# Optimization experiments

Hardware: AMD Instinct MI355X
Metric: run time of the kernel (lower is better)

Reference implementation:

```python
import jax, jax.numpy as jnp
import numpy as np

N = 50000
E = 1_600_000
IN_C, HID_C, OUT_C = 128, 64, 16
NEG_SLOPE = 0.2


def setup_inputs() -> dict:
    key = jax.random.key(0)
    ks = jax.random.split(key, 16)
    x = jax.random.normal(ks[0], (N, IN_C), dtype=jnp.float32)
    edge_index = jax.random.randint(ks[1], (2, E), 0, N, dtype=jnp.int32)
    edge_weight = jax.random.uniform(ks[2], (E,), dtype=jnp.float32)

    def lin(k, fan_in, fan_out):
        s = (6.0 / (fan_in + fan_out)) ** 0.5
        return jax.random.uniform(k, (fan_in, fan_out), jnp.float32, -s, s)

    params = {
        "W1": lin(ks[3], IN_C, HID_C),
        "a_src1": jax.random.normal(ks[4], (HID_C,), jnp.float32) * 0.1,
        "a_dst1": jax.random.normal(ks[5], (HID_C,), jnp.float32) * 0.1,
        "b1": jnp.zeros((HID_C,), jnp.float32),
        "W2": lin(ks[6], HID_C, HID_C),
        "a_src2": jax.random.normal(ks[7], (HID_C,), jnp.float32) * 0.1,
        "a_dst2": jax.random.normal(ks[8], (HID_C,), jnp.float32) * 0.1,
        "b2": jnp.zeros((HID_C,), jnp.float32),
        "W3": lin(ks[9], HID_C, OUT_C),
        "a_src3": jax.random.normal(ks[10], (OUT_C,), jnp.float32) * 0.1,
        "a_dst3": jax.random.normal(ks[11], (OUT_C,), jnp.float32) * 0.1,
        "b3": jnp.zeros((OUT_C,), jnp.float32),
    }
    return {"x": x, "edge_index": edge_index, "edge_weight": edge_weight, **params}


def gat_conv(x, W, a_src, a_dst, b, src, dst):
    """Single-head PyG GATConv, add_self_loops=False, eval mode."""
    h = x @ W                                    # [N, C]
    alpha_src = (h * a_src).sum(-1)              # [N]
    alpha_dst = (h * a_dst).sum(-1)              # [N]
    e = jax.nn.leaky_relu(alpha_src[src] + alpha_dst[dst], NEG_SLOPE)  # [E]
    # softmax over incoming edges of each target node
    m = jax.ops.segment_max(e, dst, num_segments=N)
    e = jnp.exp(e - m[dst])
    denom = jax.ops.segment_sum(e, dst, num_segments=N)
    alpha = e / (denom[dst] + 1e-16)             # [E]
    out = jax.ops.segment_sum(h[src] * alpha[:, None], dst, num_segments=N)
    return out + b


def reference(x, edge_index, edge_weight,
              W1, a_src1, a_dst1, b1,
              W2, a_src2, a_dst2, b2,
              W3, a_src3, a_dst3, b3):
    src, dst = edge_index[0], edge_index[1]
    # edge_weight unused: GATConv has no lin_edge (edge_dim=None)
    h = jax.nn.relu(gat_conv(x, W1, a_src1, a_dst1, b1, src, dst))
    h = jax.nn.relu(gat_conv(h, W2, a_src2, a_dst2, b2, src, dst))
    return gat_conv(h, W3, a_src3, a_dst3, b3, src, dst)
```

## Files before the change

kernel.cpp:

```cpp
#include <hip/hip_runtime.h>
#include <hip/hip_fp16.h>
#include <math.h>

#define N_NODES 50000
#define N_EDGES 1600000
#define BSH 8
#define NBUCK ((N_NODES + 255) >> BSH)
#define EPB 2048
#define NBLK ((N_EDGES + EPB - 1) / EPB)


__global__ __launch_bounds__(256) void bucket_hist(const int* __restrict__ dst,
                                                   int* __restrict__ bhist_t, int e) {
    __shared__ int h[NBUCK];
    for (int i = threadIdx.x; i < NBUCK; i += 256) h[i] = 0;
    __syncthreads();
    int base = blockIdx.x * EPB;
#pragma unroll
    for (int j = 0; j < EPB / 256; ++j) {
        int i = base + j * 256 + threadIdx.x;
        if (i < e) atomicAdd(&h[dst[i] >> BSH], 1);
    }
    __syncthreads();
    for (int i = threadIdx.x; i < NBUCK; i += 256)
        bhist_t[i * NBLK + blockIdx.x] = h[i];
}

__global__ __launch_bounds__(256) void bucket_totals(const int* __restrict__ bhist_t,
                                                     int* __restrict__ btot) {
    int b = blockIdx.x;
    const int* col = bhist_t + (size_t)b * NBLK;
    int s = 0;
    for (int i = threadIdx.x; i < NBLK; i += 256) s += col[i];
#pragma unroll
    for (int off = 1; off < 64; off <<= 1) s += __shfl_xor(s, off);
    __shared__ int red[4];
    if ((threadIdx.x & 63) == 0) red[threadIdx.x >> 6] = s;
    __syncthreads();
    if (threadIdx.x == 0)
        btot[b] = red[0] + red[1] + red[2] + red[3];
}

__global__ __launch_bounds__(64) void rewrite_offsets(int* __restrict__ bhist_t,
                                                      const int* __restrict__ btot,
                                                      int* __restrict__ rowptr) {
    int b = blockIdx.x;
    int lane = threadIdx.x;
    int pre = 0;
    for (int i = lane; i < NBUCK; i += 64) if (i < b) pre += btot[i];
#pragma unroll
    for (int off = 1; off < 64; off <<= 1) pre += __shfl_xor(pre, off);
    if (b == 0 && lane == 0) rowptr[N_NODES] = N_EDGES;

    int* col = bhist_t + (size_t)b * NBLK;
    __shared__ int buf[NBLK];
    for (int i = lane; i < NBLK; i += 64) buf[i] = col[i];
    __syncthreads();
    constexpr int CH = (NBLK + 63) / 64;
    int lo = lane * CH;
    int hi = lo + CH; if (hi > NBLK) hi = NBLK;
    int s = 0;
    for (int i = lo; i < hi; ++i) s += buf[i];
    int inc = s;
#pragma unroll
    for (int off = 1; off < 64; off <<= 1) {
        int t = __shfl_up(inc, off);
        if (lane >= off) inc += t;
    }
    int run = pre + inc - s;
    for (int i = lo; i < hi; ++i) { int c = buf[i]; col[i] = run; run += c; }
}

__global__ __launch_bounds__(256) void bucket_scatter(const int* __restrict__ src,
                                                      const int* __restrict__ dst,
                                                      const int* __restrict__ bhist_t,
                                                      unsigned* __restrict__ packed, int e) {
    __shared__ int lcnt[NBUCK];
    __shared__ int lbase[NBUCK];
    __shared__ int gbase[NBUCK];
    __shared__ unsigned stage[EPB];
    __shared__ unsigned char sbk[EPB];
    __shared__ int wsum[4];
    int r = blockIdx.x;
    for (int i = threadIdx.x; i < NBUCK; i += 256) {
        lcnt[i] = 0;
        gbase[i] = bhist_t[i * NBLK + r];
    }
    __syncthreads();
    int base = r * EPB;
    int bk[EPB / 256], lrank[EPB / 256];
    unsigned pk[EPB / 256];
    bool val[EPB / 256];
#pragma unroll
    for (int j = 0; j < EPB / 256; ++j) {
        int i = base + j * 256 + threadIdx.x;
        val[j] = (i < e);
        if (val[j]) {
            int d = dst[i];
            bk[j] = d >> BSH;
            pk[j] = (unsigned)src[i] | ((unsigned)(d & ((1 << BSH) - 1)) << 16);
            lrank[j] = atomicAdd(&lcnt[bk[j]], 1);
        }
    }
    __syncthreads();
    {
        int lane = threadIdx.x & 63, w = threadIdx.x >> 6;
        int v = (threadIdx.x < NBUCK) ? lcnt[threadIdx.x] : 0;
        int inc = v;
#pragma unroll
        for (int off = 1; off < 64; off <<= 1) {
            int t = __shfl_up(inc, off);
            if (lane >= off) inc += t;
        }
        if (lane == 63) wsum[w] = inc;
        __syncthreads();
        int woff = 0;
#pragma unroll
        for (int k = 0; k < 3; ++k) if (k < w) woff += wsum[k];
        if (threadIdx.x < NBUCK) lbase[threadIdx.x] = woff + inc - v;
    }
    __syncthreads();
#pragma unroll
    for (int j = 0; j < EPB / 256; ++j) {
        if (val[j]) {
            int slot = lbase[bk[j]] + lrank[j];
            stage[slot] = pk[j];
            sbk[slot] = (unsigned char)bk[j];
        }
    }
    __syncthreads();
    int vn = e - base; if (vn > EPB) vn = EPB;
    for (int i = threadIdx.x; i < vn; i += 256) {
        int b = sbk[i];
        packed[gbase[b] + (i - lbase[b])] = stage[i];
    }
}

__global__ __launch_bounds__(512) void csr_finalize(const unsigned* __restrict__ packed,
                                                    const int* __restrict__ btot,
                                                    int* __restrict__ rowptr,
                                                    unsigned short* __restrict__ csr_src) {
    int b = blockIdx.x;
    __shared__ int sb[2];
    if (threadIdx.x < 64) {
        int pre = 0, tot = 0;
        for (int i = threadIdx.x; i < NBUCK; i += 64) {
            int v = btot[i];
            if (i < b) pre += v;
            if (i == b) tot = v;
        }
#pragma unroll
        for (int off = 1; off < 64; off <<= 1) {
            pre += __shfl_xor(pre, off);
            tot += __shfl_xor(tot, off);
        }
        if (threadIdx.x == 0) { sb[0] = pre; sb[1] = pre + tot; }
    }
    __syncthreads();
    int s0 = sb[0], s1 = sb[1];
    int cnt = s1 - s0;
    __shared__ int ncnt[256];
    __shared__ int ncur[256];
    __shared__ int wsum[4];
    if (threadIdx.x < 256) ncnt[threadIdx.x] = 0;
    __syncthreads();
    for (int i = threadIdx.x; i < cnt; i += 512)
        atomicAdd(&ncnt[packed[s0 + i] >> 16], 1);
    __syncthreads();
    int lane = threadIdx.x & 63, w = threadIdx.x >> 6;
    int v = 0, inc = 0;
    if (threadIdx.x < 256) {
        v = ncnt[threadIdx.x]; inc = v;
#pragma unroll
        for (int off = 1; off < 64; off <<= 1) {
            int t = __shfl_up(inc, off);
            if (lane >= off) inc += t;
        }
        if (lane == 63) wsum[w] = inc;
    }
    __syncthreads();
    if (threadIdx.x < 256) {
        int woff = 0;
#pragma unroll
        for (int k = 0; k < 3; ++k) if (k < w) woff += wsum[k];
        int excl = woff + inc - v;
        int node = (b << BSH) + threadIdx.x;
        if (node < N_NODES) rowptr[node] = s0 + excl;
        ncur[threadIdx.x] = s0 + excl;
    }
    __syncthreads();
    for (int i = threadIdx.x; i < cnt; i += 512) {
        unsigned p = packed[s0 + i];
        int pos = atomicAdd(&ncur[p >> 16], 1);
        csr_src[pos] = (unsigned short)(p & 0xFFFFu);
    }
}


template<int K, int C, bool IN_HALF, bool OUT_HALF>
__global__ __launch_bounds__(256) void gemm_alpha(
        const void* __restrict__ inv, const float* __restrict__ W,
        const float* __restrict__ a_src, const float* __restrict__ a_dst,
        void* __restrict__ hv, float* __restrict__ as_, float* __restrict__ ad_, int n)
{
    constexpr int CPT = C / 16;
    constexpr int KP = K + 4;
    __shared__ float sx[64][KP];
    __shared__ float sW[K * C];
    int row0 = blockIdx.x * 64;
    int nvalid = n - row0;

    if constexpr (IN_HALF) {
        const __half* inh = (const __half*)inv;
        for (int idx = threadIdx.x; idx < 64 * K / 8; idx += 256) {
            int r = idx / (K / 8), kc = idx % (K / 8);
            uint4 v = {0u, 0u, 0u, 0u};
            if (r < nvalid) v = *(const uint4*)&inh[(size_t)(row0 + r) * K + kc * 8];
            float2 f0 = __half22float2(*(__half2*)&v.x);
            float2 f1 = __half22float2(*(__half2*)&v.y);
            float2 f2 = __half22float2(*(__half2*)&v.z);
            float2 f3 = __half22float2(*(__half2*)&v.w);
            float* d = &sx[r][kc * 8];
            d[0] = f0.x; d[1] = f0.y; d[2] = f1.x; d[3] = f1.y;
            d[4] = f2.x; d[5] = f2.y; d[6] = f3.x; d[7] = f3.y;
        }
    } else {
        const float* in = (const float*)inv;
        for (int idx = threadIdx.x; idx < 64 * K / 4; idx += 256) {
            int r = idx / (K / 4), kc = idx % (K / 4);
            float4 v = {0, 0, 0, 0};
            if (r < nvalid) v = *(const float4*)&in[(size_t)(row0 + r) * K + kc * 4];
            *(float4*)&sx[r][kc * 4] = v;
        }
    }
    for (int idx = threadIdx.x; idx < K * C / 4; idx += 256)
        *(float4*)&sW[idx * 4] = *(const float4*)&W[idx * 4];
    __syncthreads();

    int g  = threadIdx.x >> 4;
    int ci = threadIdx.x & 15;
    int r0 = g * 4;
    int c0 = ci * CPT;

    if constexpr (CPT == 4) {
        float4 acc0 = {0,0,0,0}, acc1 = {0,0,0,0}, acc2 = {0,0,0,0}, acc3 = {0,0,0,0};
        for (int k = 0; k < K; k += 4) {
            float4 w0 = *(const float4*)&sW[(k + 0) * C + c0];
            float4 w1 = *(const float4*)&sW[(k + 1) * C + c0];
            float4 w2 = *(const float4*)&sW[(k + 2) * C + c0];
            float4 w3 = *(const float4*)&sW[(k + 3) * C + c0];
            float4 x0 = *(const float4*)&sx[r0 + 0][k];
            float4 x1 = *(const float4*)&sx[r0 + 1][k];
            float4 x2 = *(const float4*)&sx[r0 + 2][k];
            float4 x3 = *(const float4*)&sx[r0 + 3][k];
#define STEP(A, X) \
            A.x = fmaf(X.x, w0.x, A.x); A.y = fmaf(X.x, w0.y, A.y); \
            A.z = fmaf(X.x, w0.z, A.z); A.w = fmaf(X.x, w0.w, A.w); \
            A.x = fmaf(X.y, w1.x, A.x); A.y = fmaf(X.y, w1.y, A.y); \
            A.z = fmaf(X.y, w1.z, A.z); A.w = fmaf(X.y, w1.w, A.w); \
            A.x = fmaf(X.z, w2.x, A.x); A.y = fmaf(X.z, w2.y, A.y); \
            A.z = fmaf(X.z, w2.z, A.z); A.w = fmaf(X.z, w2.w, A.w); \
            A.x = fmaf(X.w, w3.x, A.x); A.y = fmaf(X.w, w3.y, A.y); \
            A.z = fmaf(X.w, w3.z, A.z); A.w = fmaf(X.w, w3.w, A.w);
            STEP(acc0, x0) STEP(acc1, x1) STEP(acc2, x2) STEP(acc3, x3)
#undef STEP
        }
        if constexpr (OUT_HALF) {
            __half* hh = (__half*)hv;
            auto sth = [&](int r, float4 a) {
                if (r0 + r < nvalid) {
                    size_t base = (size_t)(row0 + r0 + r) * C + c0;
                    *(__half2*)&hh[base]     = __floats2half2_rn(a.x, a.y);
                    *(__half2*)&hh[base + 2] = __floats2half2_rn(a.z, a.w);
                }
            };
            sth(0, acc0); sth(1, acc1); sth(2, acc2); sth(3, acc3);
        } else {
            float* h = (float*)hv;
            if (r0 + 0 < nvalid) *(float4*)&h[(size_t)(row0 + r0 + 0) * C + c0] = acc0;
            if (r0 + 1 < nvalid) *(float4*)&h[(size_t)(row0 + r0 + 1) * C + c0] = acc1;
            if (r0 + 2 < nvalid) *(float4*)&h[(size_t)(row0 + r0 + 2) * C + c0] = acc2;
            if (r0 + 3 < nvalid) *(float4*)&h[(size_t)(row0 + r0 + 3) * C + c0] = acc3;
        }
        float4 asv = *(const float4*)&a_src[c0];
        float4 adv = *(const float4*)&a_dst[c0];
        float vs0 = acc0.x*asv.x + acc0.y*asv.y + acc0.z*asv.z + acc0.w*asv.w;
        float vs1 = acc1.x*asv.x + acc1.y*asv.y + acc1.z*asv.z + acc1.w*asv.w;
        float vs2 = acc2.x*asv.x + acc2.y*asv.y + acc2.z*asv.z + acc2.w*asv.w;
        float vs3 = acc3.x*asv.x + acc3.y*asv.y + acc3.z*asv.z + acc3.w*asv.w;
        float vd0 = acc0.x*adv.x + acc0.y*adv.y + acc0.z*adv.z + acc0.w*adv.w;
        float vd1 = acc1.x*adv.x + acc1.y*adv.y + acc1.z*adv.z + acc1.w*adv.w;
        float vd2 = acc2.x*adv.x + acc2.y*adv.y + acc2.z*adv.z + acc2.w*adv.w;
        float vd3 = acc3.x*adv.x + acc3.y*adv.y + acc3.z*adv.z + acc3.w*adv.w;
#pragma unroll
        for (int off = 1; off < 16; off <<= 1) {
            vs0 += __shfl_xor(vs0, off); vs1 += __shfl_xor(vs1, off);
            vs2 += __shfl_xor(vs2, off); vs3 += __shfl_xor(vs3, off);
            vd0 += __shfl_xor(vd0, off); vd1 += __shfl_xor(vd1, off);
            vd2 += __shfl_xor(vd2, off); vd3 += __shfl_xor(vd3, off);
        }
        if (ci == 0) {
            if (r0 + 0 < nvalid) { as_[row0+r0+0] = vs0; ad_[row0+r0+0] = vd0; }
            if (r0 + 1 < nvalid) { as_[row0+r0+1] = vs1; ad_[row0+r0+1] = vd1; }
            if (r0 + 2 < nvalid) { as_[row0+r0+2] = vs2; ad_[row0+r0+2] = vd2; }
            if (r0 + 3 < nvalid) { as_[row0+r0+3] = vs3; ad_[row0+r0+3] = vd3; }
        }
    } else {
        float s0 = 0.f, s1 = 0.f, s2 = 0.f, s3 = 0.f;
        for (int k = 0; k < K; k += 4) {
            float w0 = sW[(k + 0) * C + c0];
            float w1 = sW[(k + 1) * C + c0];
            float w2 = sW[(k + 2) * C + c0];
            float w3 = sW[(k + 3) * C + c0];
            float4 x0 = *(const float4*)&sx[r0 + 0][k];
            float4 x1 = *(const float4*)&sx[r0 + 1][k];
            float4 x2 = *(const float4*)&sx[r0 + 2][k];
            float4 x3 = *(const float4*)&sx[r0 + 3][k];
            s0 = fmaf(x0.x,w0, fmaf(x0.y,w1, fmaf(x0.z,w2, fmaf(x0.w,w3, s0))));
            s1 = fmaf(x1.x,w0, fmaf(x1.y,w1, fmaf(x1.z,w2, fmaf(x1.w,w3, s1))));
            s2 = fmaf(x2.x,w0, fmaf(x2.y,w1, fmaf(x2.z,w2, fmaf(x2.w,w3, s2))));
            s3 = fmaf(x3.x,w0, fmaf(x3.y,w1, fmaf(x3.z,w2, fmaf(x3.w,w3, s3))));
        }
        if constexpr (OUT_HALF) {
            __half* hh = (__half*)hv;
            if (r0 + 0 < nvalid) hh[(size_t)(row0+r0+0) * C + c0] = __float2half_rn(s0);
            if (r0 + 1 < nvalid) hh[(size_t)(row0+r0+1) * C + c0] = __float2half_rn(s1);
            if (r0 + 2 < nvalid) hh[(size_t)(row0+r0+2) * C + c0] = __float2half_rn(s2);
            if (r0 + 3 < nvalid) hh[(size_t)(row0+r0+3) * C + c0] = __float2half_rn(s3);
        } else {
            float* h = (float*)hv;
            if (r0 + 0 < nvalid) h[(size_t)(row0+r0+0) * C + c0] = s0;
            if (r0 + 1 < nvalid) h[(size_t)(row0+r0+1) * C + c0] = s1;
            if (r0 + 2 < nvalid) h[(size_t)(row0+r0+2) * C + c0] = s2;
            if (r0 + 3 < nvalid) h[(size_t)(row0+r0+3) * C + c0] = s3;
        }
        float as0 = a_src[c0], ad0 = a_dst[c0];
        float vs0 = s0*as0, vs1 = s1*as0, vs2 = s2*as0, vs3 = s3*as0;
        float vd0 = s0*ad0, vd1 = s1*ad0, vd2 = s2*ad0, vd3 = s3*ad0;
#pragma unroll
        for (int off = 1; off < 16; off <<= 1) {
            vs0 += __shfl_xor(vs0, off); vs1 += __shfl_xor(vs1, off);
            vs2 += __shfl_xor(vs2, off); vs3 += __shfl_xor(vs3, off);
            vd0 += __shfl_xor(vd0, off); vd1 += __shfl_xor(vd1, off);
            vd2 += __shfl_xor(vd2, off); vd3 += __shfl_xor(vd3, off);
        }
        if (ci == 0) {
            if (r0 + 0 < nvalid) { as_[row0+r0+0] = vs0; ad_[row0+r0+0] = vd0; }
            if (r0 + 1 < nvalid) { as_[row0+r0+1] = vs1; ad_[row0+r0+1] = vd1; }
            if (r0 + 2 < nvalid) { as_[row0+r0+2] = vs2; ad_[row0+r0+2] = vd2; }
            if (r0 + 3 < nvalid) { as_[row0+r0+3] = vs3; ad_[row0+r0+3] = vd3; }
        }
    }
}


__device__ __forceinline__ float leaky(float e) {
    return (e >= 0.f) ? e : 0.2f * e;
}

__device__ __forceinline__ void hacc8(uint4 r, float w, float4& accL, float4& accH) {
    float2 f0 = __half22float2(*(__half2*)&r.x);
    float2 f1 = __half22float2(*(__half2*)&r.y);
    float2 f2 = __half22float2(*(__half2*)&r.z);
    float2 f3 = __half22float2(*(__half2*)&r.w);
    accL.x = fmaf(w, f0.x, accL.x); accL.y = fmaf(w, f0.y, accL.y);
    accL.z = fmaf(w, f1.x, accL.z); accL.w = fmaf(w, f1.y, accL.w);
    accH.x = fmaf(w, f2.x, accH.x); accH.y = fmaf(w, f2.y, accH.y);
    accH.z = fmaf(w, f3.x, accH.z); accH.w = fmaf(w, f3.y, accH.w);
}

template<bool RELU>
__global__ __launch_bounds__(256) void agg64h(
        const __half* __restrict__ h, const float* __restrict__ as_, const float* __restrict__ ad_,
        const int* __restrict__ rowptr, const unsigned short* __restrict__ csr_src,
        const float* __restrict__ bias, __half* __restrict__ out, int n)
{
    int node = (blockIdx.x * blockDim.x + threadIdx.x) >> 6;
    if (node >= n) return;
    int lane = threadIdx.x & 63;
    int g  = lane >> 3;
    int c8 = lane & 7;
    int start = rowptr[node], end = rowptr[node + 1];
    float adn = ad_[node];
    const char* hb = (const char*)h + (size_t)c8 * 16;

    float4 accL = {0,0,0,0}, accH = {0,0,0,0};
    float dsum = 0.f;

    for (int chunk = start; chunk < end; chunk += 64) {
        int e_i = chunk + lane;
        int soff = 0; float aw = 0.f;
        if (e_i < end) {
            int ssrc = csr_src[e_i];
            soff = ssrc << 7;
            aw = __expf(leaky(as_[ssrc] + adn));
        }
        dsum += aw;
        int nv = end - chunk; if (nv > 64) nv = 64;
        int nvu = (nv + 31) & ~31;
        for (int j = g; j < nvu; j += 32) {
            int   o0 = __shfl(soff, j),      o1 = __shfl(soff, j + 8);
            int   o2 = __shfl(soff, j + 16), o3 = __shfl(soff, j + 24);
            float w0 = __shfl(aw, j),        w1 = __shfl(aw, j + 8);
            float w2 = __shfl(aw, j + 16),   w3 = __shfl(aw, j + 24);
            uint4 r0 = *(const uint4*)(hb + o0);
            uint4 r1 = *(const uint4*)(hb + o1);
            uint4 r2 = *(const uint4*)(hb + o2);
            uint4 r3 = *(const uint4*)(hb + o3);
            hacc8(r0, w0, accL, accH); hacc8(r1, w1, accL, accH);
            hacc8(r2, w2, accL, accH); hacc8(r3, w3, accL, accH);
        }
    }
#pragma unroll
    for (int off = 8; off <= 32; off <<= 1) {
        accL.x += __shfl_xor(accL.x, off); accL.y += __shfl_xor(accL.y, off);
        accL.z += __shfl_xor(accL.z, off); accL.w += __shfl_xor(accL.w, off);
        accH.x += __shfl_xor(accH.x, off); accH.y += __shfl_xor(accH.y, off);
        accH.z += __shfl_xor(accH.z, off); accH.w += __shfl_xor(accH.w, off);
    }
#pragma unroll
    for (int off = 1; off <= 32; off <<= 1) dsum += __shfl_xor(dsum, off);

    if (g == 0) {
        float inv = 1.f / (dsum + 1e-16f);
        float4 bl = *(const float4*)&bias[c8 * 8];
        float4 bh = *(const float4*)&bias[c8 * 8 + 4];
        float4 ol, oh;
        ol.x = fmaf(accL.x, inv, bl.x); ol.y = fmaf(accL.y, inv, bl.y);
        ol.z = fmaf(accL.z, inv, bl.z); ol.w = fmaf(accL.w, inv, bl.w);
        oh.x = fmaf(accH.x, inv, bh.x); oh.y = fmaf(accH.y, inv, bh.y);
        oh.z = fmaf(accH.z, inv, bh.z); oh.w = fmaf(accH.w, inv, bh.w);
        if (RELU) {
            ol.x = fmaxf(ol.x, 0.f); ol.y = fmaxf(ol.y, 0.f);
            ol.z = fmaxf(ol.z, 0.f); ol.w = fmaxf(ol.w, 0.f);
            oh.x = fmaxf(oh.x, 0.f); oh.y = fmaxf(oh.y, 0.f);
            oh.z = fmaxf(oh.z, 0.f); oh.w = fmaxf(oh.w, 0.f);
        }
        __half2 p0 = __floats2half2_rn(ol.x, ol.y);
        __half2 p1 = __floats2half2_rn(ol.z, ol.w);
        __half2 p2 = __floats2half2_rn(oh.x, oh.y);
        __half2 p3 = __floats2half2_rn(oh.z, oh.w);
        uint4 pk;
        pk.x = *(unsigned*)&p0; pk.y = *(unsigned*)&p1;
        pk.z = *(unsigned*)&p2; pk.w = *(unsigned*)&p3;
        *(uint4*)&out[(size_t)node * 64 + c8 * 8] = pk;
    }
}

template<bool RELU>
__global__ __launch_bounds__(256) void agg16h(
        const __half* __restrict__ h, const float* __restrict__ as_, const float* __restrict__ ad_,
        const int* __restrict__ rowptr, const unsigned short* __restrict__ csr_src,
        const float* __restrict__ bias, float* __restrict__ out, int n)
{
    int node = (blockIdx.x * blockDim.x + threadIdx.x) >> 6;
    if (node >= n) return;
    int lane = threadIdx.x & 63;
    int g   = lane >> 1;
    int c16 = lane & 1;
    int start = rowptr[node], end = rowptr[node + 1];
    float adn = ad_[node];
    const char* hb = (const char*)h + (size_t)c16 * 16;

    float4 accL = {0,0,0,0}, accH = {0,0,0,0};
    float dsum = 0.f;

    for (int chunk = start; chunk < end; chunk += 64) {
        int e_i = chunk + lane;
        int soff = 0; float aw = 0.f;
        if (e_i < end) {
            int ssrc = csr_src[e_i];
            soff = ssrc << 5;
            aw = __expf(leaky(as_[ssrc] + adn));
        }
        dsum += aw;
        int nv = end - chunk; if (nv > 64) nv = 64;
        int nvu = (nv + 31) & ~31;
        for (int j = g; j < nvu; j += 32) {
            int   o0 = __shfl(soff, j);
            float w0 = __shfl(aw, j);
            uint4 r0 = *(const uint4*)(hb + o0);
            hacc8(r0, w0, accL, accH);
        }
    }
#pragma unroll
    for (int off = 2; off <= 32; off <<= 1) {
        accL.x += __shfl_xor(accL.x, off); accL.y += __shfl_xor(accL.y, off);
        accL.z += __shfl_xor(accL.z, off); accL.w += __shfl_xor(accL.w, off);
        accH.x += __shfl_xor(accH.x, off); accH.y += __shfl_xor(accH.y, off);
        accH.z += __shfl_xor(accH.z, off); accH.w += __shfl_xor(accH.w, off);
    }
#pragma unroll
    for (int off = 1; off <= 32; off <<= 1) dsum += __shfl_xor(dsum, off);

    if (g == 0) {
        float inv = 1.f / (dsum + 1e-16f);
        float4 bl = *(const float4*)&bias[c16 * 8];
        float4 bh = *(const float4*)&bias[c16 * 8 + 4];
        float4 ol, oh;
        ol.x = fmaf(accL.x, inv, bl.x); ol.y = fmaf(accL.y, inv, bl.y);
        ol.z = fmaf(accL.z, inv, bl.z); ol.w = fmaf(accL.w, inv, bl.w);
        oh.x = fmaf(accH.x, inv, bh.x); oh.y = fmaf(accH.y, inv, bh.y);
        oh.z = fmaf(accH.z, inv, bh.z); oh.w = fmaf(accH.w, inv, bh.w);
        if (RELU) {
            ol.x = fmaxf(ol.x, 0.f); ol.y = fmaxf(ol.y, 0.f);
            ol.z = fmaxf(ol.z, 0.f); ol.w = fmaxf(ol.w, 0.f);
            oh.x = fmaxf(oh.x, 0.f); oh.y = fmaxf(oh.y, 0.f);
            oh.z = fmaxf(oh.z, 0.f); oh.w = fmaxf(oh.w, 0.f);
        }
        *(float4*)&out[(size_t)node * 16 + c16 * 8]     = ol;
        *(float4*)&out[(size_t)node * 16 + c16 * 8 + 4] = oh;
    }
}


extern "C" void kernel_launch(void* const* d_in, const int* in_sizes, int n_in,
                              void* d_out, int out_size, void* d_ws, size_t ws_size,
                              hipStream_t stream) {
    const float* x   = (const float*)d_in[0];
    const int*   ei  = (const int*)  d_in[1];
    const float* W1  = (const float*)d_in[3];
    const float* as1 = (const float*)d_in[4];
    const float* ad1 = (const float*)d_in[5];
    const float* b1  = (const float*)d_in[6];
    const float* W2  = (const float*)d_in[7];
    const float* as2 = (const float*)d_in[8];
    const float* ad2 = (const float*)d_in[9];
    const float* b2  = (const float*)d_in[10];
    const float* W3  = (const float*)d_in[11];
    const float* as3 = (const float*)d_in[12];
    const float* ad3 = (const float*)d_in[13];
    const float* b3  = (const float*)d_in[14];

    const int* srcp = ei;
    const int* dstp = ei + N_EDGES;

    char* ws = (char*)d_ws;
    size_t off = 0;
    auto alloc = [&](size_t bytes) -> void* {
        void* p = ws + off;
        off = (off + bytes + 255) & ~(size_t)255;
        return p;
    };
    int*   bhist_t = (int*)   alloc((size_t)NBUCK * NBLK * sizeof(int));
    int*   btot    = (int*)   alloc(NBUCK * sizeof(int));
    int*   rowptr  = (int*)   alloc((N_NODES + 1) * sizeof(int));
    unsigned short* csr_src = (unsigned short*)alloc((size_t)N_EDGES * sizeof(unsigned short));
    float* asb     = (float*) alloc(N_NODES * sizeof(float));
    float* adb     = (float*) alloc(N_NODES * sizeof(float));
    __half* hHalf  = (__half*)alloc((size_t)N_NODES * 64 * sizeof(__half));
    __half* aHalf  = (__half*)alloc((size_t)N_NODES * 64 * sizeof(__half));
    __half* h16    = (__half*)alloc((size_t)N_NODES * 16 * sizeof(__half));
    unsigned* packed = (unsigned*)alloc((size_t)N_EDGES * sizeof(unsigned));

    bucket_hist    <<<NBLK,  256, 0, stream>>>(dstp, bhist_t, N_EDGES);
    bucket_totals  <<<NBUCK, 256, 0, stream>>>(bhist_t, btot);
    rewrite_offsets<<<NBUCK, 64,  0, stream>>>(bhist_t, btot, rowptr);
    bucket_scatter <<<NBLK,  256, 0, stream>>>(srcp, dstp, bhist_t, packed, N_EDGES);
    csr_finalize   <<<NBUCK, 512, 0, stream>>>(packed, btot, rowptr, csr_src);

    const int NB64 = (N_NODES + 63) / 64;
    const int NB4  = (N_NODES + 3) / 4;

    gemm_alpha<128, 64, false, true><<<NB64, 256, 0, stream>>>(x, W1, as1, ad1, hHalf, asb, adb, N_NODES);
    agg64h<true><<<NB4, 256, 0, stream>>>(hHalf, asb, adb, rowptr, csr_src, b1, aHalf, N_NODES);

    gemm_alpha<64, 64, true, true><<<NB64, 256, 0, stream>>>(aHalf, W2, as2, ad2, hHalf, asb, adb, N_NODES);
    agg64h<true><<<NB4, 256, 0, stream>>>(hHalf, asb, adb, rowptr, csr_src, b2, aHalf, N_NODES);

    gemm_alpha<64, 16, true, true><<<NB64, 256, 0, stream>>>(aHalf, W3, as3, ad3, h16, asb, adb, N_NODES);
    agg16h<false><<<NB4, 256, 0, stream>>>(h16, asb, adb, rowptr, csr_src, b3, (float*)d_out, N_NODES);
}
```

Before: 184.4 us.

## Fuse CSR build stages into one cooperative kernel with grid syncs

Replaces the five CSR construction kernels (histogram, totals, offset rewrite, scatter, finalize) with a single cooperative kernel that uses grid-wide syncs between phases. Each block keeps its edges, bucket ids and local ranks in registers across phases, so the dst array is no longer re-read and four kernel launch gaps disappear. The trade-off is that all 782 blocks of 256 threads must be co-resident for the cooperative launch, grid.sync has its own cost, and the finalize phase now runs with 256 threads per bucket instead of 512.

```diff
diff --git a/kernel.cpp b/kernel.cpp
--- a/kernel.cpp
+++ b/kernel.cpp
@@ -1,6 +1,9 @@
 #include <hip/hip_runtime.h>
 #include <hip/hip_fp16.h>
+#include <hip/hip_cooperative_groups.h>
 #include <math.h>
+
+namespace cg = cooperative_groups;
 
 #define N_NODES 50000
 #define N_EDGES 1600000
@@ -8,101 +11,46 @@
 #define NBUCK ((N_NODES + 255) >> BSH)
 #define EPB 2048
 #define NBLK ((N_EDGES + EPB - 1) / EPB)
-
-
-__global__ __launch_bounds__(256) void bucket_hist(const int* __restrict__ dst,
-                                                   int* __restrict__ bhist_t, int e) {
-    __shared__ int h[NBUCK];
-    for (int i = threadIdx.x; i < NBUCK; i += 256) h[i] = 0;
-    __syncthreads();
-    int base = blockIdx.x * EPB;
-#pragma unroll
-    for (int j = 0; j < EPB / 256; ++j) {
-        int i = base + j * 256 + threadIdx.x;
-        if (i < e) atomicAdd(&h[dst[i] >> BSH], 1);
-    }
-    __syncthreads();
-    for (int i = threadIdx.x; i < NBUCK; i += 256)
-        bhist_t[i * NBLK + blockIdx.x] = h[i];
-}
-
-__global__ __launch_bounds__(256) void bucket_totals(const int* __restrict__ bhist_t,
-                                                     int* __restrict__ btot) {
-    int b = blockIdx.x;
-    const int* col = bhist_t + (size_t)b * NBLK;
-    int s = 0;
-    for (int i = threadIdx.x; i < NBLK; i += 256) s += col[i];
-#pragma unroll
-    for (int off = 1; off < 64; off <<= 1) s += __shfl_xor(s, off);
-    __shared__ int red[4];
-    if ((threadIdx.x & 63) == 0) red[threadIdx.x >> 6] = s;
-    __syncthreads();
-    if (threadIdx.x == 0)
-        btot[b] = red[0] + red[1] + red[2] + red[3];
-}
-
-__global__ __launch_bounds__(64) void rewrite_offsets(int* __restrict__ bhist_t,
-                                                      const int* __restrict__ btot,
-                                                      int* __restrict__ rowptr) {
-    int b = blockIdx.x;
-    int lane = threadIdx.x;
-    int pre = 0;
-    for (int i = lane; i < NBUCK; i += 64) if (i < b) pre += btot[i];
-#pragma unroll
-    for (int off = 1; off < 64; off <<= 1) pre += __shfl_xor(pre, off);
-    if (b == 0 && lane == 0) rowptr[N_NODES] = N_EDGES;
-
-    int* col = bhist_t + (size_t)b * NBLK;
-    __shared__ int buf[NBLK];
-    for (int i = lane; i < NBLK; i += 64) buf[i] = col[i];
-    __syncthreads();
-    constexpr int CH = (NBLK + 63) / 64;
-    int lo = lane * CH;
-    int hi = lo + CH; if (hi > NBLK) hi = NBLK;
-    int s = 0;
-    for (int i = lo; i < hi; ++i) s += buf[i];
-    int inc = s;
-#pragma unroll
-    for (int off = 1; off < 64; off <<= 1) {
-        int t = __shfl_up(inc, off);
-        if (lane >= off) inc += t;
-    }
-    int run = pre + inc - s;
-    for (int i = lo; i < hi; ++i) { int c = buf[i]; col[i] = run; run += c; }
-}
-
-__global__ __launch_bounds__(256) void bucket_scatter(const int* __restrict__ src,
-                                                      const int* __restrict__ dst,
-                                                      const int* __restrict__ bhist_t,
-                                                      unsigned* __restrict__ packed, int e) {
+#define EPT (EPB / 256)
+
+
+__global__ __launch_bounds__(256) void csr_build(
+        const int* __restrict__ src, const int* __restrict__ dst,
+        int* __restrict__ bhist_t, int* __restrict__ btot,
+        int* __restrict__ rowptr, unsigned* __restrict__ packed,
+        unsigned short* __restrict__ csr_src)
+{
+    cg::grid_group grid = cg::this_grid();
+    int r = blockIdx.x;
     __shared__ int lcnt[NBUCK];
     __shared__ int lbase[NBUCK];
     __shared__ int gbase[NBUCK];
     __shared__ unsigned stage[EPB];
     __shared__ unsigned char sbk[EPB];
+    __shared__ int ncnt[256];
+    __shared__ int ncur[256];
     __shared__ int wsum[4];
-    int r = blockIdx.x;
-    for (int i = threadIdx.x; i < NBUCK; i += 256) {
-        lcnt[i] = 0;
-        gbase[i] = bhist_t[i * NBLK + r];
-    }
+
+    for (int i = threadIdx.x; i < NBUCK; i += 256) lcnt[i] = 0;
     __syncthreads();
     int base = r * EPB;
-    int bk[EPB / 256], lrank[EPB / 256];
-    unsigned pk[EPB / 256];
-    bool val[EPB / 256];
-#pragma unroll
-    for (int j = 0; j < EPB / 256; ++j) {
+    int bk[EPT], lrank[EPT];
+    unsigned pk[EPT];
+    bool val[EPT];
+#pragma unroll
+    for (int j = 0; j < EPT; ++j) {
         int i = base + j * 256 + threadIdx.x;
-        val[j] = (i < e);
+        val[j] = (i < N_EDGES);
         if (val[j]) {
             int d = dst[i];
             bk[j] = d >> BSH;
             pk[j] = (unsigned)src[i] | ((unsigned)(d & ((1 << BSH) - 1)) << 16);
             lrank[j] = atomicAdd(&lcnt[bk[j]], 1);
-        }
+        } else { bk[j] = 0; pk[j] = 0u; lrank[j] = 0; }
     }
     __syncthreads();
+    for (int i = threadIdx.x; i < NBUCK; i += 256)
+        bhist_t[i * NBLK + r] = lcnt[i];
     {
         int lane = threadIdx.x & 63, w = threadIdx.x >> 6;
         int v = (threadIdx.x < NBUCK) ? lcnt[threadIdx.x] : 0;
@@ -119,9 +67,55 @@
         for (int k = 0; k < 3; ++k) if (k < w) woff += wsum[k];
         if (threadIdx.x < NBUCK) lbase[threadIdx.x] = woff + inc - v;
     }
+    grid.sync();
+
+    if (r < NBUCK) {
+        const int* col = bhist_t + (size_t)r * NBLK;
+        int s = 0;
+        for (int i = threadIdx.x; i < NBLK; i += 256) s += col[i];
+#pragma unroll
+        for (int off = 1; off < 64; off <<= 1) s += __shfl_xor(s, off);
+        if ((threadIdx.x & 63) == 0) wsum[threadIdx.x >> 6] = s;
+        __syncthreads();
+        if (threadIdx.x == 0)
+            btot[r] = wsum[0] + wsum[1] + wsum[2] + wsum[3];
+    }
+    grid.sync();
+
+    if (r < NBUCK) {
+        if (threadIdx.x < 64) {
+            int lane = threadIdx.x;
+            int pre = 0;
+            for (int i = lane; i < NBUCK; i += 64) if (i < r) pre += btot[i];
+#pragma unroll
+            for (int off = 1; off < 64; off <<= 1) pre += __shfl_xor(pre, off);
+            if (r == 0 && lane == 0) rowptr[N_NODES] = N_EDGES;
+
+            int* col = bhist_t + (size_t)r * NBLK;
+            int* buf = (int*)stage;
+            for (int i = lane; i < NBLK; i += 64) buf[i] = col[i];
+            constexpr int CH = (NBLK + 63) / 64;
+            int lo = lane * CH;
+            int hi = lo + CH; if (hi > NBLK) hi = NBLK;
+            int s = 0;
+            for (int i = lo; i < hi; ++i) s += buf[i];
+            int inc = s;
+#pragma unroll
+            for (int off = 1; off < 64; off <<= 1) {
+                int t = __shfl_up(inc, off);
+                if (lane >= off) inc += t;
+            }
+            int run = pre + inc - s;
+            for (int i = lo; i < hi; ++i) { int c = buf[i]; col[i] = run; run += c; }
+        }
+    }
+    grid.sync();
+
+    for (int i = threadIdx.x; i < NBUCK; i += 256)
+        gbase[i] = bhist_t[i * NBLK + r];
     __syncthreads();
 #pragma unroll
-    for (int j = 0; j < EPB / 256; ++j) {
+    for (int j = 0; j < EPT; ++j) {
         if (val[j]) {
             int slot = lbase[bk[j]] + lrank[j];
             stage[slot] = pk[j];
@@ -129,70 +123,61 @@
         }
     }
     __syncthreads();
-    int vn = e - base; if (vn > EPB) vn = EPB;
+    int vn = N_EDGES - base; if (vn > EPB) vn = EPB;
     for (int i = threadIdx.x; i < vn; i += 256) {
         int b = sbk[i];
         packed[gbase[b] + (i - lbase[b])] = stage[i];
     }
-}
-
-__global__ __launch_bounds__(512) void csr_finalize(const unsigned* __restrict__ packed,
-                                                    const int* __restrict__ btot,
-                                                    int* __restrict__ rowptr,
-                                                    unsigned short* __restrict__ csr_src) {
-    int b = blockIdx.x;
-    __shared__ int sb[2];
-    if (threadIdx.x < 64) {
-        int pre = 0, tot = 0;
-        for (int i = threadIdx.x; i < NBUCK; i += 64) {
-            int v = btot[i];
-            if (i < b) pre += v;
-            if (i == b) tot = v;
-        }
-#pragma unroll
-        for (int off = 1; off < 64; off <<= 1) {
-            pre += __shfl_xor(pre, off);
-            tot += __shfl_xor(tot, off);
-        }
-        if (threadIdx.x == 0) { sb[0] = pre; sb[1] = pre + tot; }
-    }
-    __syncthreads();
-    int s0 = sb[0], s1 = sb[1];
-    int cnt = s1 - s0;
-    __shared__ int ncnt[256];
-    __shared__ int ncur[256];
-    __shared__ int wsum[4];
-    if (threadIdx.x < 256) ncnt[threadIdx.x] = 0;
-    __syncthreads();
-    for (int i = threadIdx.x; i < cnt; i += 512)
-        atomicAdd(&ncnt[packed[s0 + i] >> 16], 1);
-    __syncthreads();
-    int lane = threadIdx.x & 63, w = threadIdx.x >> 6;
-    int v = 0, inc = 0;
-    if (threadIdx.x < 256) {
-        v = ncnt[threadIdx.x]; inc = v;
+    grid.sync();
+
+    if (r < NBUCK) {
+        int s0 = 0, tot = 0;
+        {
+            if (threadIdx.x < 64) {
+                int pre = 0, t = 0;
+                for (int i = threadIdx.x; i < NBUCK; i += 64) {
+                    int v = btot[i];
+                    if (i < r) pre += v;
+                    if (i == r) t = v;
+                }
+#pragma unroll
+                for (int off = 1; off < 64; off <<= 1) {
+                    pre += __shfl_xor(pre, off);
+                    t += __shfl_xor(t, off);
+                }
+                if (threadIdx.x == 0) { wsum[0] = pre; wsum[1] = t; }
+            }
+            __syncthreads();
+            s0 = wsum[0]; tot = wsum[1];
+        }
+        int cnt = tot;
+        if (threadIdx.x < 256) ncnt[threadIdx.x] = 0;
+        __syncthreads();
+        for (int i = threadIdx.x; i < cnt; i += 256)
+            atomicAdd(&ncnt[packed[s0 + i] >> 16], 1);
+        __syncthreads();
+        int lane = threadIdx.x & 63, w = threadIdx.x >> 6;
+        int v = ncnt[threadIdx.x], inc = v;
 #pragma unroll
         for (int off = 1; off < 64; off <<= 1) {
             int t = __shfl_up(inc, off);
             if (lane >= off) inc += t;
         }
         if (lane == 63) wsum[w] = inc;
-    }
-    __syncthreads();
-    if (threadIdx.x < 256) {
+        __syncthreads();
         int woff = 0;
 #pragma unroll
         for (int k = 0; k < 3; ++k) if (k < w) woff += wsum[k];
         int excl = woff + inc - v;
-        int node = (b << BSH) + threadIdx.x;
+        int node = (r << BSH) + threadIdx.x;
         if (node < N_NODES) rowptr[node] = s0 + excl;
         ncur[threadIdx.x] = s0 + excl;
-    }
-    __syncthreads();
-    for (int i = threadIdx.x; i < cnt; i += 512) {
-        unsigned p = packed[s0 + i];
-        int pos = atomicAdd(&ncur[p >> 16], 1);
-        csr_src[pos] = (unsigned short)(p & 0xFFFFu);
+        __syncthreads();
+        for (int i = threadIdx.x; i < cnt; i += 256) {
+            unsigned p = packed[s0 + i];
+            int pos = atomicAdd(&ncur[p >> 16], 1);
+            csr_src[pos] = (unsigned short)(p & 0xFFFFu);
+        }
     }
 }
 
@@ -440,10 +425,10 @@
         __half2 p1 = __floats2half2_rn(ol.z, ol.w);
         __half2 p2 = __floats2half2_rn(oh.x, oh.y);
         __half2 p3 = __floats2half2_rn(oh.z, oh.w);
-        uint4 pk;
-        pk.x = *(unsigned*)&p0; pk.y = *(unsigned*)&p1;
-        pk.z = *(unsigned*)&p2; pk.w = *(unsigned*)&p3;
-        *(uint4*)&out[(size_t)node * 64 + c8 * 8] = pk;
+        uint4 pkv;
+        pkv.x = *(unsigned*)&p0; pkv.y = *(unsigned*)&p1;
+        pkv.z = *(unsigned*)&p2; pkv.w = *(unsigned*)&p3;
+        *(uint4*)&out[(size_t)node * 64 + c8 * 8] = pkv;
     }
 }
 
@@ -553,11 +538,12 @@
     __half* h16    = (__half*)alloc((size_t)N_NODES * 16 * sizeof(__half));
     unsigned* packed = (unsigned*)alloc((size_t)N_EDGES * sizeof(unsigned));
 
-    bucket_hist    <<<NBLK,  256, 0, stream>>>(dstp, bhist_t, N_EDGES);
-    bucket_totals  <<<NBUCK, 256, 0, stream>>>(bhist_t, btot);
-    rewrite_offsets<<<NBUCK, 64,  0, stream>>>(bhist_t, btot, rowptr);
-    bucket_scatter <<<NBLK,  256, 0, stream>>>(srcp, dstp, bhist_t, packed, N_EDGES);
-    csr_finalize   <<<NBUCK, 512, 0, stream>>>(packed, btot, rowptr, csr_src);
+    {
+        void* args[] = { (void*)&srcp, (void*)&dstp, (void*)&bhist_t, (void*)&btot,
+                         (void*)&rowptr, (void*)&packed, (void*)&csr_src };
+        hipLaunchCooperativeKernel((void*)csr_build, dim3(NBLK), dim3(256),
+                                   args, 0, stream);
+    }
 
     const int NB64 = (N_NODES + 63) / 64;
     const int NB4  = (N_NODES + 3) / 4;
```

Measured after the change: 532.8 us. 189% more time.
